# Kernel tuning notes

Measured on AMD Instinct MI355X. Metric: run time of the kernel, lower is better.

Reference implementation:

```python
import jax, jax.numpy as jnp
from jax import lax
import numpy as np

B, Tf, C, D = 4, 128, 8, 64     # batch, frames (num_tokens), animals, input_dim
E, H, L, O = 512, 8, 6, 256     # n_embd, n_head, n_layer, output_dim
T = Tf * C                      # sequence length = 1024
DH = E // H
EPS = 1e-5


def _ln(x, g, b):
    m = jnp.mean(x, -1, keepdims=True)
    v = jnp.mean((x - m) ** 2, -1, keepdims=True)
    return (x - m) * lax.rsqrt(v + EPS) * g + b


def setup_inputs():
    key = jax.random.key(0)
    ks = jax.random.split(key, 16)
    s = 0.02
    n = lambda k, sh: jax.random.normal(k, sh, jnp.float32) * s
    z = lambda sh: jnp.zeros(sh, jnp.float32)
    o = lambda sh: jnp.ones(sh, jnp.float32)
    return {
        'tokens': jax.random.normal(ks[0], (B, Tf, C, D), jnp.float32),
        'pos': (jnp.arange(B * T) % T).reshape(B, T),
        'mask': o((B, T)),
        'bn_g': o((D,)), 'bn_b': z((D,)),
        'We': n(ks[1], (D, E)), 'be': z((E,)),
        'ln1_g': o((L, E)), 'ln1_b': z((L, E)),
        'ln2_g': o((L, E)), 'ln2_b': z((L, E)),
        'Wq': n(ks[2], (L, E, E)), 'bq': z((L, E)),
        'Wk': n(ks[3], (L, E, E)), 'bk': z((L, E)),
        'Wv': n(ks[4], (L, E, E)), 'bv': z((L, E)),
        'Wo': n(ks[5], (L, E, E)), 'bo': z((L, E)),
        'W1': n(ks[6], (L, E, 4 * E)), 'b1': z((L, 4 * E)),
        'W2': n(ks[7], (L, 4 * E, E)), 'b2': z((L, E)),
        'lnf_g': o((E,)), 'lnf_b': z((E,)),
        'Wp': n(ks[8], (E, O)), 'bp': z((O,)),
        'Wd1': n(ks[9], (O, O)), 'bd1': z((O,)),
        'lnd_g': o((O,)), 'lnd_b': z((O,)),
        'Wd2': n(ks[10], (O, D)), 'bd2': z((D,)),
        'Wf1': n(ks[11], (O, O)), 'bf1': z((O,)),
        'lnfr_g': o((O,)), 'lnfr_b': z((O,)),
        'Wf2': n(ks[12], (O, D * C)), 'bf2': z((D * C,)),
    }


def _forward(tokens, mask, bn_g, bn_b, We, be, ln1_g, ln1_b, ln2_g, ln2_b,
             Wq, bq, Wk, bk, Wv, bv, Wo, bo, W1, b1, W2, b2,
             lnf_g, lnf_b, Wp, bp, Wd1, bd1, lnd_g, lnd_b, Wd2, bd2,
             Wf1, bf1, lnfr_g, lnfr_b, Wf2, bf2):
    # BatchNorm2d over feature channel D (training-mode batch stats, biased var)
    mu = jnp.mean(tokens, axis=(0, 1, 2))
    var = jnp.mean((tokens - mu) ** 2, axis=(0, 1, 2))
    tn = (tokens - mu) * lax.rsqrt(var + EPS) * bn_g + bn_b
    x0 = (tn @ We + be).reshape(B, T, E)  # token embeddings, [B,T,E]

    # static block-causal mask: causal over frames, all-to-all within a frame
    static = jnp.kron(jnp.tril(jnp.ones((Tf, Tf), jnp.float32)),
                      jnp.ones((C, C), jnp.float32))  # [T,T]

    def run_blocks(x, dyn):  # dyn: [B,T] key-mask
        allow = (static[None, None] * dyn[:, None, None, :]) > 0  # [B,1,T,T]

        def step(x, p):
            l1g, l1b, wq, bq_, wk, bk_, wv, bv_, wo, bo_, l2g, l2b, w1, b1_, w2, b2_ = p
            h = _ln(x, l1g, l1b)
            q = (h @ wq + bq_).reshape(B, T, H, DH)
            k = (h @ wk + bk_).reshape(B, T, H, DH)
            v = (h @ wv + bv_).reshape(B, T, H, DH)
            att = jnp.einsum('bthd,bshd->bhts', q, k) / jnp.sqrt(jnp.float32(DH))
            att = jnp.where(allow, att, -jnp.inf)
            att = jax.nn.softmax(att, axis=-1)
            y = jnp.einsum('bhts,bshd->bthd', att, v).reshape(B, T, E)
            x = x + y @ wo + bo_
            h2 = _ln(x, l2g, l2b)
            x = x + jax.nn.gelu(h2 @ w1 + b1_, approximate=False) @ w2 + b2_
            return x, None

        x, _ = lax.scan(step, x, (ln1_g, ln1_b, Wq, bq, Wk, bk, Wv, bv, Wo, bo,
                                  ln2_g, ln2_b, W1, b1, W2, b2))
        return x

    x = run_blocks(x0, mask)
    x = _ln(x, lnf_g, lnf_b) @ Wp + bp                 # [B,T,O]
    x2 = run_blocks(x0[:, ::-1], mask[:, ::-1])
    x2 = _ln(x2, lnf_g, lnf_b) @ Wp + bp

    toks = tokens.reshape(B, T, D) * mask[:, :, None]

    def decoder(z):
        h = jnp.tanh(z @ Wd1 + bd1)
        return _ln(h, lnd_g, lnd_b) @ Wd2 + bd2

    def frame_decoder(z):
        h = jnp.tanh(z @ Wf1 + bf1)
        return _ln(h, lnfr_g, lnfr_b) @ Wf2 + bf2

    mse = lambda a, b_: jnp.mean((a - b_) ** 2)
    pred = decoder(x) * mask[:, :, None]
    l_reg = mse(pred[:, :-C], toks[:, C:])
    pred2 = decoder(x2) * mask[:, :, None]
    l_reg_rl = mse(pred2[:, :-C], toks[:, ::-1][:, C:])

    xf = x.reshape(B, Tf, C, O).mean(axis=-2)          # [B,Tf,O]
    l_fr_lr = mse(frame_decoder(xf)[:, :-1], toks.reshape(B, Tf, C * D)[:, 1:])
    xf2 = x2.reshape(B, Tf, C, O).mean(axis=-2)
    l_fr_rl = mse(frame_decoder(xf2)[:, :-1], toks.reshape(B, Tf, C * D)[:, ::-1][:, 1:])

    losses = jnp.stack([l_reg, l_reg_rl, l_fr_lr, l_fr_rl])
    return xf, losses


def reference(tokens, pos, mask, bn_g, bn_b, We, be, ln1_g, ln1_b, ln2_g, ln2_b,
              Wq, bq, Wk, bk, Wv, bv, Wo, bo, W1, b1, W2, b2,
              lnf_g, lnf_b, Wp, bp, Wd1, bd1, lnd_g, lnd_b, Wd2, bd2,
              Wf1, bf1, lnfr_g, lnfr_b, Wf2, bf2):
    # pos is accepted but unused, matching the original forward
    return _forward(tokens, mask, bn_g, bn_b, We, be, ln1_g, ln1_b, ln2_g, ln2_b,
                    Wq, bq, Wk, bk, Wv, bv, Wo, bo, W1, b1, W2, b2,
                    lnf_g, lnf_b, Wp, bp, Wd1, bd1, lnd_g, lnd_b, Wd2, bd2,
                    Wf1, bf1, lnfr_g, lnfr_b, Wf2, bf2)
```

## Files before the change

### kernel.cpp

```cpp
#include <hip/hip_runtime.h>
#include <math.h>

typedef short short8 __attribute__((ext_vector_type(8)));
typedef float f32x4 __attribute__((ext_vector_type(4)));

__device__ __forceinline__ float block_reduce(float v, float* red) {
  int tid = threadIdx.x;
  red[tid] = v; __syncthreads();
  for (int s = 128; s >= 1; s >>= 1) {
    if (tid < s) red[tid] += red[tid + s];
    __syncthreads();
  }
  float r = red[0];
  __syncthreads();
  return r;
}

__device__ __forceinline__ void cvt1(float x, unsigned short& h, unsigned short& l) {
  unsigned u = __float_as_uint(x);
  unsigned hb = (u + 0x8000u) & 0xffff0000u;
  h = (unsigned short)(hb >> 16);
  l = (unsigned short)(__float_as_uint(x - __uint_as_float(hb)) >> 16);
}

__device__ __forceinline__ void cvt2(float a, float b, unsigned& hp, unsigned& lp) {
  unsigned ua = __float_as_uint(a), ub = __float_as_uint(b);
  unsigned ha = (ua + 0x8000u) & 0xffff0000u;
  unsigned hb = (ub + 0x8000u) & 0xffff0000u;
  float la = a - __uint_as_float(ha);
  float lb = b - __uint_as_float(hb);
  hp = (ha >> 16) | hb;
  lp = (__float_as_uint(la) >> 16) | (__float_as_uint(lb) & 0xffff0000u);
}

__device__ __forceinline__ void gl2l(const unsigned short* g, unsigned short* l) {
  __builtin_amdgcn_global_load_lds(
      (const __attribute__((address_space(1))) void*)g,
      (__attribute__((address_space(3))) void*)l, 16, 0, 0);
}

union U8 { unsigned u[4]; short8 s; };

__global__ __launch_bounds__(256) void sentinel_kernel(float* __restrict__ out, int n, float v) {
  int i = blockIdx.x * 256 + threadIdx.x;
  if (i < n) out[i] = v;
}

__global__ __launch_bounds__(256) void bn_stats_kernel(
    const float* __restrict__ tok, const float* __restrict__ g,
    const float* __restrict__ bb, float* __restrict__ ss) {
  __shared__ float red[256];
  const int d = blockIdx.x;
  float sum = 0.f, sumsq = 0.f;
  for (int s = threadIdx.x; s < 4096; s += 256) {
    float v = tok[s * 64 + d];
    sum += v; sumsq += v * v;
  }
  sum = block_reduce(sum, red);
  sumsq = block_reduce(sumsq, red);
  if (threadIdx.x == 0) {
    float mu = sum * (1.f / 4096.f);
    float var = sumsq * (1.f / 4096.f) - mu * mu;
    float sc = g[d] * rsqrtf(fmaxf(var, 0.f) + 1e-5f);
    ss[d] = sc;
    ss[64 + d] = bb[d] - mu * sc;
  }
}

__global__ __launch_bounds__(256) void tn_kernel(
    const float* __restrict__ tok, const float* __restrict__ ss,
    float* __restrict__ tn) {
  int idx = blockIdx.x * 256 + threadIdx.x;
  int d = idx & 63;
  tn[idx] = tok[idx] * ss[d] + ss[64 + d];
}

__global__ __launch_bounds__(256) void reverse_kernel(
    const float* __restrict__ x0, float* __restrict__ x0r) {
  int idx = blockIdx.x * 256 + threadIdx.x;
  int row = idx >> 9, e = idx & 511;
  int b = row >> 10, t = row & 1023;
  x0r[idx] = x0[((size_t)((b << 10) + (1023 - t))) * 512 + e];
}

__global__ __launch_bounds__(256) void ln_kernel(
    const float* __restrict__ x, const float* __restrict__ g,
    const float* __restrict__ b, float* __restrict__ out, int N) {
  __shared__ float red[256];
  const size_t r = blockIdx.x;
  const int tid = threadIdx.x;
  float v0 = x[r * N + tid];
  float v1 = (N > 256) ? x[r * N + 256 + tid] : 0.f;
  float sum = block_reduce(v0 + v1, red);
  float sumsq = block_reduce(v0 * v0 + v1 * v1, red);
  float mean = sum / (float)N;
  float var = sumsq / (float)N - mean * mean;
  float rs = rsqrtf(fmaxf(var, 0.f) + 1e-5f);
  out[r * N + tid] = (v0 - mean) * rs * g[tid] + b[tid];
  if (N > 256)
    out[r * N + 256 + tid] = (v1 - mean) * rs * g[256 + tid] + b[256 + tid];
}

__global__ __launch_bounds__(256) void ln_pl(
    const float* __restrict__ x, const float* __restrict__ g,
    const float* __restrict__ b, unsigned short* __restrict__ oh,
    unsigned short* __restrict__ ol) {
  __shared__ float red[256];
  const size_t r = blockIdx.x;
  const int tid = threadIdx.x;
  float v0 = x[r * 512 + tid];
  float v1 = x[r * 512 + 256 + tid];
  float sum = block_reduce(v0 + v1, red);
  float sumsq = block_reduce(v0 * v0 + v1 * v1, red);
  float mean = sum * (1.f / 512.f);
  float var = sumsq * (1.f / 512.f) - mean * mean;
  float rs = rsqrtf(fmaxf(var, 0.f) + 1e-5f);
  float o0 = (v0 - mean) * rs * g[tid] + b[tid];
  float o1 = (v1 - mean) * rs * g[256 + tid] + b[256 + tid];
  unsigned short h0, l0, h1, l1;
  cvt1(o0, h0, l0); cvt1(o1, h1, l1);
  oh[r * 512 + tid] = h0;       ol[r * 512 + tid] = l0;
  oh[r * 512 + 256 + tid] = h1; ol[r * 512 + 256 + tid] = l1;
}

__global__ __launch_bounds__(256) void convw(
    const float* __restrict__ W, unsigned short* __restrict__ hi,
    unsigned short* __restrict__ lo, int K, int N, long dls) {
  int id = blockIdx.x * 256 + threadIdx.x;
  int total = (K >> 3) * N;
  if (id >= total) return;
  int c = id / N, n = id - c * N;
  const float* Wp = W + (size_t)blockIdx.y * K * N;
  size_t doff = (size_t)blockIdx.y * dls + (size_t)n * K + c * 8;
  unsigned short h8[8], l8[8];
#pragma unroll
  for (int j = 0; j < 8; ++j) {
    float xv = Wp[(size_t)(c * 8 + j) * N + n];
    cvt1(xv, h8[j], l8[j]);
  }
  uint4 hv = make_uint4(h8[0] | ((unsigned)h8[1] << 16), h8[2] | ((unsigned)h8[3] << 16),
                        h8[4] | ((unsigned)h8[5] << 16), h8[6] | ((unsigned)h8[7] << 16));
  uint4 lv = make_uint4(l8[0] | ((unsigned)l8[1] << 16), l8[2] | ((unsigned)l8[3] << 16),
                        l8[4] | ((unsigned)l8[5] << 16), l8[6] | ((unsigned)l8[7] << 16));
  *reinterpret_cast<uint4*>(hi + doff) = hv;
  *reinterpret_cast<uint4*>(lo + doff) = lv;
}

#define BK 16
template <int ACT>
__global__ __launch_bounds__(256) void gemm3(
    const float* __restrict__ A, const float* __restrict__ W,
    const float* __restrict__ bias, const float* resid,
    float* out, int M, int N, int K) {
  __shared__ float As[BK][64 + 4];
  __shared__ float Bs[BK][64 + 4];
  const int tid = threadIdx.x;
  const int tx = tid & 15, ty = tid >> 4;
  const int n0 = blockIdx.x * 64, m0 = blockIdx.y * 64;
  float acc[4][4] = {};
  for (int k0 = 0; k0 < K; k0 += BK) {
    {
      int m = tid >> 2, kq = tid & 3;
      float4 a4 = *reinterpret_cast<const float4*>(A + (size_t)(m0 + m) * K + k0 + kq * 4);
      As[kq * 4 + 0][m] = a4.x; As[kq * 4 + 1][m] = a4.y;
      As[kq * 4 + 2][m] = a4.z; As[kq * 4 + 3][m] = a4.w;
    }
    {
      int kk = tid >> 4, nq = tid & 15;
      float4 b4 = *reinterpret_cast<const float4*>(W + (size_t)(k0 + kk) * N + n0 + nq * 4);
      Bs[kk][nq * 4 + 0] = b4.x; Bs[kk][nq * 4 + 1] = b4.y;
      Bs[kk][nq * 4 + 2] = b4.z; Bs[kk][nq * 4 + 3] = b4.w;
    }
    __syncthreads();
#pragma unroll
    for (int kq = 0; kq < BK; ++kq) {
      float4 av = *reinterpret_cast<const float4*>(&As[kq][ty * 4]);
      float4 bv = *reinterpret_cast<const float4*>(&Bs[kq][tx * 4]);
      acc[0][0] += av.x * bv.x; acc[0][1] += av.x * bv.y; acc[0][2] += av.x * bv.z; acc[0][3] += av.x * bv.w;
      acc[1][0] += av.y * bv.x; acc[1][1] += av.y * bv.y; acc[1][2] += av.y * bv.z; acc[1][3] += av.y * bv.w;
      acc[2][0] += av.z * bv.x; acc[2][1] += av.z * bv.y; acc[2][2] += av.z * bv.z; acc[2][3] += av.z * bv.w;
      acc[3][0] += av.w * bv.x; acc[3][1] += av.w * bv.y; acc[3][2] += av.w * bv.z; acc[3][3] += av.w * bv.w;
    }
    __syncthreads();
  }
#pragma unroll
  for (int i = 0; i < 4; ++i) {
    int m = m0 + ty * 4 + i;
#pragma unroll
    for (int j = 0; j < 4; ++j) {
      int n = n0 + tx * 4 + j;
      float v = acc[i][j] + bias[n];
      if (resid) v += resid[(size_t)m * N + n];
      if (ACT == 1) v = 0.5f * v * (1.f + erff(v * 0.70710678118654752f));
      if (ACT == 2) v = tanhf(v);
      out[(size_t)m * N + n] = v;
    }
  }
}

template <int ACT, int OUTMODE, int ATOMIC, int BIAS3, int QKV>
__global__ __launch_bounds__(256, 2) void gemm_bf(
    const unsigned short* __restrict__ Ahp, const unsigned short* __restrict__ Alp,
    const unsigned short* __restrict__ Bhp, const unsigned short* __restrict__ Blp,
    const float* __restrict__ b0, const float* __restrict__ b1, const float* __restrict__ b2,
    float* __restrict__ Cf, unsigned short* __restrict__ Chp, unsigned short* __restrict__ Clp,
    unsigned short* __restrict__ vth, unsigned short* __restrict__ vtl,
    int M, int N, int K, int KZ) {
  __shared__ __align__(16) unsigned short LDS[2][4][128][32];
  const int tid = threadIdx.x;
  const int lane = tid & 63, wid = tid >> 6;
  const int wr = wid >> 1, wc = wid & 1;
  const int lr = lane & 15, lq = lane >> 4;

  const int gx = gridDim.x;
  int lin = blockIdx.y * gx + blockIdx.x;
  int qch = (gx * gridDim.y) >> 3;
  int swz = (lin & 7) * qch + (lin >> 3);
  const int nb = swz % gx, mb = swz / gx;
  const int n0 = nb * 128, m0 = mb * 128;
  const int kbase = blockIdx.z * KZ, kend = kbase + KZ;

  f32x4 acc[4][4];
#pragma unroll
  for (int i = 0; i < 4; ++i)
#pragma unroll
    for (int j = 0; j < 4; ++j) { acc[i][j][0] = 0.f; acc[i][j][1] = 0.f; acc[i][j][2] = 0.f; acc[i][j][3] = 0.f; }

  const unsigned short* gplane =
      (wid == 0) ? Ahp + (size_t)m0 * K :
      (wid == 1) ? Alp + (size_t)m0 * K :
      (wid == 2) ? Bhp + (size_t)n0 * K : Blp + (size_t)n0 * K;
  const int srow = lane >> 2;
  const int sphys = lane & 3;

  auto stage = [&](int buf, int k0) {
#pragma unroll
    for (int j = 0; j < 8; ++j) {
      int row = j * 16 + srow;
      int logslot = sphys ^ ((row >> 1) & 3);
      gl2l(gplane + (size_t)row * K + k0 + logslot * 8, &LDS[buf][wid][j * 16][0]);
    }
  };

  stage(0, kbase);
  __syncthreads();
  int cur = 0;
  for (int k0 = kbase; k0 < kend; k0 += 32) {
    if (k0 + 32 < kend) stage(cur ^ 1, k0 + 32);
    short8 ah[4], al[4], bh[4], bl[4];
#pragma unroll
    for (int mi = 0; mi < 4; ++mi) {
      int row = wr * 64 + mi * 16 + lr;
      int off = (lq ^ ((row >> 1) & 3)) * 8;
      ah[mi] = *reinterpret_cast<const short8*>(&LDS[cur][0][row][off]);
      al[mi] = *reinterpret_cast<const short8*>(&LDS[cur][1][row][off]);
    }
#pragma unroll
    for (int ni = 0; ni < 4; ++ni) {
      int n = wc * 64 + ni * 16 + lr;
      int off = (lq ^ ((n >> 1) & 3)) * 8;
      bh[ni] = *reinterpret_cast<const short8*>(&LDS[cur][2][n][off]);
      bl[ni] = *reinterpret_cast<const short8*>(&LDS[cur][3][n][off]);
    }
#pragma unroll
    for (int mi = 0; mi < 4; ++mi)
#pragma unroll
      for (int ni = 0; ni < 4; ++ni) {
        acc[mi][ni] = __builtin_amdgcn_mfma_f32_16x16x32_bf16(ah[mi], bh[ni], acc[mi][ni], 0, 0, 0);
        acc[mi][ni] = __builtin_amdgcn_mfma_f32_16x16x32_bf16(ah[mi], bl[ni], acc[mi][ni], 0, 0, 0);
        acc[mi][ni] = __builtin_amdgcn_mfma_f32_16x16x32_bf16(al[mi], bh[ni], acc[mi][ni], 0, 0, 0);
      }
    __syncthreads();
    cur ^= 1;
  }

  if (QKV) {
    const float* bsec = (n0 < 512) ? b0 : (n0 < 1024 ? b1 : b2);
    const int bof = (n0 & 511) - n0;
    if (n0 < 1024) {
      const float scale = (n0 < 512) ? 0.125f : 1.f;
#pragma unroll
      for (int mi = 0; mi < 4; ++mi)
#pragma unroll
        for (int r = 0; r < 4; ++r) {
          int grow = m0 + wr * 64 + mi * 16 + lq * 4 + r;
#pragma unroll
          for (int ni = 0; ni < 4; ++ni) {
            int col = n0 + wc * 64 + ni * 16 + lr;
            float v = (acc[mi][ni][r] + bsec[col + bof]) * scale;
            unsigned short hv, lv;
            cvt1(v, hv, lv);
            Chp[(size_t)grow * N + col] = hv;
            Clp[(size_t)grow * N + col] = lv;
          }
        }
    } else {
#pragma unroll
      for (int mi = 0; mi < 4; ++mi) {
        int t0 = m0 + wr * 64 + mi * 16 + lq * 4;
        int bb = t0 >> 10, tt = t0 & 1023;
#pragma unroll
        for (int ni = 0; ni < 4; ++ni) {
          int col = n0 + wc * 64 + ni * 16 + lr;
          float bias = bsec[col + bof];
          int hh_ = (col - 1024) >> 6, dd = (col - 1024) & 63;
          unsigned short h4[4], l4[4];
#pragma unroll
          for (int r = 0; r < 4; ++r) cvt1(acc[mi][ni][r] + bias, h4[r], l4[r]);
          size_t off = ((size_t)((bb * 8 + hh_) * 64 + dd)) * 1024 + tt;
          *reinterpret_cast<uint2*>(vth + off) = make_uint2(
              h4[0] | ((unsigned)h4[1] << 16), h4[2] | ((unsigned)h4[3] << 16));
          *reinterpret_cast<uint2*>(vtl + off) = make_uint2(
              l4[0] | ((unsigned)l4[1] << 16), l4[2] | ((unsigned)l4[3] << 16));
        }
      }
    }
    return;
  }
  const float* bsec = b0;
  int bof = 0;
  if (BIAS3) { bsec = (n0 < 512) ? b0 : (n0 < 1024 ? b1 : b2); bof = (n0 & 511) - n0; }
#pragma unroll
  for (int mi = 0; mi < 4; ++mi) {
#pragma unroll
    for (int r = 0; r < 4; ++r) {
      int grow = m0 + wr * 64 + mi * 16 + lq * 4 + r;
#pragma unroll
      for (int ni = 0; ni < 4; ++ni) {
        int col = n0 + wc * 64 + ni * 16 + lr;
        float v = acc[mi][ni][r];
        float bias = BIAS3 ? bsec[col + bof] : b0[col];
        if (ATOMIC) {
          if (blockIdx.z == 0) v += bias;
          atomicAdd(&Cf[(size_t)grow * N + col], v);
        } else {
          v += bias;
          if (ACT == 1) v = 0.5f * v * (1.f + erff(v * 0.70710678118654752f));
          if (ACT == 2) v = tanhf(v);
          if (OUTMODE == 0 || OUTMODE == 2) Cf[(size_t)grow * N + col] = v;
          if (OUTMODE >= 1) {
            unsigned short hv, lv;
            cvt1(v, hv, lv);
            Chp[(size_t)grow * N + col] = hv;
            Clp[(size_t)grow * N + col] = lv;
          }
        }
      }
    }
  }
}

__global__ __launch_bounds__(256, 3) void attn_mfma(
    const unsigned short* __restrict__ qkvh, const unsigned short* __restrict__ qkvl,
    const unsigned short* __restrict__ vth, const unsigned short* __restrict__ vtl,
    const float* __restrict__ mask,
    unsigned short* __restrict__ ybh, unsigned short* __restrict__ ybl, int rev) {
  __shared__ __align__(16) unsigned short QK[2][4096];
  __shared__ __align__(16) unsigned short VT[2][4096];
  __shared__ float PU[64 * 68];
  __shared__ float km[64];

  const int tid = threadIdx.x;
  const int lane = tid & 63, w = tid >> 6;
  const int lr = lane & 15, lq = lane >> 4;

  const int id = blockIdx.x;
  const int top = id >> 8;
  const int r5 = id & 255;
  const int qt = top ? (15 - (r5 >> 4)) : (r5 >> 4);
  const int bh_ = (r5 & 15) | (top << 4);
  const int b = bh_ >> 3, h = bh_ & 7;

  {
    const unsigned short* src = (w < 2) ? qkvh : qkvl;
    unsigned short* dst = QK[w >> 1];
    int half = w & 1;
#pragma unroll
    for (int j = 0; j < 4; ++j) {
      int chunk = half * 256 + j * 64 + lane;
      int row = chunk >> 3, p = chunk & 7;
      int slot = p ^ (row & 7);
      gl2l(src + (size_t)(b * 1024 + qt * 64 + row) * 1536 + h * 64 + slot * 8,
           dst + (half * 256 + j * 64) * 8);
    }
  }
  __syncthreads();
  short8 qa_h[2], qa_l[2];
#pragma unroll
  for (int ks = 0; ks < 2; ++ks) {
    int row = w * 16 + lr;
    int phys = (lq + ks * 4) ^ (row & 7);
    qa_h[ks] = *reinterpret_cast<const short8*>(&QK[0][row * 64 + phys * 8]);
    qa_l[ks] = *reinterpret_cast<const short8*>(&QK[1][row * 64 + phys * 8]);
  }
  __syncthreads();

  float m_[4], l_[4] = {0.f, 0.f, 0.f, 0.f};
  f32x4 o_[4];
#pragma unroll
  for (int r = 0; r < 4; ++r) m_[r] = -1e30f;
#pragma unroll
  for (int df = 0; df < 4; ++df) { o_[df][0] = 0.f; o_[df][1] = 0.f; o_[df][2] = 0.f; o_[df][3] = 0.f; }

  for (int kt = 0; kt <= qt; ++kt) {
    if (w < 2) {
      const unsigned short* src = (w == 0) ? qkvh : qkvl;
      unsigned short* dst = QK[w];
#pragma unroll
      for (int j = 0; j < 8; ++j) {
        int chunk = j * 64 + lane;
        int row = chunk >> 3, p = chunk & 7;
        int slot = p ^ (row & 7);
        gl2l(src + (size_t)(b * 1024 + kt * 64 + row) * 1536 + 512 + h * 64 + slot * 8,
             dst + j * 512);
      }
    } else {
      const unsigned short* src = (w == 2) ? vth : vtl;
      unsigned short* dst = VT[w - 2];
#pragma unroll
      for (int j = 0; j < 8; ++j) {
        int chunk = j * 64 + lane;
        int row = chunk >> 3, p = chunk & 7;
        int slot = p ^ (row & 7);
        gl2l(src + (size_t)((b * 8 + h) * 64 + row) * 1024 + kt * 64 + slot * 8,
             dst + j * 512);
      }
    }
    if (tid < 64) {
      int s = kt * 64 + tid;
      km[tid] = mask[b * 1024 + (rev ? (1023 - s) : s)];
    }
    __syncthreads();

    f32x4 sacc[4];
#pragma unroll
    for (int kf = 0; kf < 4; ++kf) { sacc[kf][0] = 0.f; sacc[kf][1] = 0.f; sacc[kf][2] = 0.f; sacc[kf][3] = 0.f; }
#pragma unroll
    for (int ks = 0; ks < 2; ++ks) {
#pragma unroll
      for (int kf = 0; kf < 4; ++kf) {
        int col = kf * 16 + lr;
        int phys = (lq + ks * 4) ^ (lr & 7);
        short8 kbh = *reinterpret_cast<const short8*>(&QK[0][col * 64 + phys * 8]);
        short8 kbl = *reinterpret_cast<const short8*>(&QK[1][col * 64 + phys * 8]);
        sacc[kf] = __builtin_amdgcn_mfma_f32_16x16x32_bf16(qa_h[ks], kbh, sacc[kf], 0, 0, 0);
        sacc[kf] = __builtin_amdgcn_mfma_f32_16x16x32_bf16(qa_h[ks], kbl, sacc[kf], 0, 0, 0);
        sacc[kf] = __builtin_amdgcn_mfma_f32_16x16x32_bf16(qa_l[ks], kbh, sacc[kf], 0, 0, 0);
      }
    }

    const bool diag = (kt == qt);
    float kmv[4];
#pragma unroll
    for (int kf = 0; kf < 4; ++kf) kmv[kf] = km[kf * 16 + lr];
#pragma unroll
    for (int r = 0; r < 4; ++r) {
      int fi = (w * 16 + lq * 4 + r) >> 3;
      float mt = -1e30f;
#pragma unroll
      for (int kf = 0; kf < 4; ++kf) {
        int key = kf * 16 + lr;
        bool ok = (kmv[kf] > 0.f) && (!diag || ((key >> 3) <= fi));
        float x = ok ? sacc[kf][r] : -1e30f;
        sacc[kf][r] = x;
        mt = fmaxf(mt, x);
      }
      mt = fmaxf(mt, __shfl_xor(mt, 1, 16));
      mt = fmaxf(mt, __shfl_xor(mt, 2, 16));
      mt = fmaxf(mt, __shfl_xor(mt, 4, 16));
      mt = fmaxf(mt, __shfl_xor(mt, 8, 16));
      float mn = fmaxf(m_[r], mt);
      float al = __expf(m_[r] - mn);
      m_[r] = mn;
      float rs = 0.f;
#pragma unroll
      for (int kf = 0; kf < 4; ++kf) {
        float sv = sacc[kf][r];
        float p = (sv > -1e29f) ? __expf(sv - mn) : 0.f;
        sacc[kf][r] = p;
        rs += p;
      }
      rs += __shfl_xor(rs, 1, 16);
      rs += __shfl_xor(rs, 2, 16);
      rs += __shfl_xor(rs, 4, 16);
      rs += __shfl_xor(rs, 8, 16);
      l_[r] = l_[r] * al + rs;
#pragma unroll
      for (int df = 0; df < 4; ++df) o_[df][r] *= al;
    }
#pragma unroll
    for (int kf = 0; kf < 4; ++kf)
#pragma unroll
      for (int r = 0; r < 4; ++r)
        PU[(w * 16 + lq * 4 + r) * 68 + kf * 16 + lr] = sacc[kf][r];
    __syncthreads();

#pragma unroll
    for (int ks = 0; ks < 2; ++ks) {
      const float* pp = &PU[(w * 16 + lr) * 68 + ks * 32 + lq * 8];
      float4 p0 = *reinterpret_cast<const float4*>(pp);
      float4 p1 = *reinterpret_cast<const float4*>(pp + 4);
      U8 th, tl;
      cvt2(p0.x, p0.y, th.u[0], tl.u[0]);
      cvt2(p0.z, p0.w, th.u[1], tl.u[1]);
      cvt2(p1.x, p1.y, th.u[2], tl.u[2]);
      cvt2(p1.z, p1.w, th.u[3], tl.u[3]);
      short8 pa_h = th.s, pa_l = tl.s;
#pragma unroll
      for (int df = 0; df < 4; ++df) {
        int col = df * 16 + lr;
        int phys = (lq + ks * 4) ^ (lr & 7);
        short8 vbh = *reinterpret_cast<const short8*>(&VT[0][col * 64 + phys * 8]);
        short8 vbl = *reinterpret_cast<const short8*>(&VT[1][col * 64 + phys * 8]);
        o_[df] = __builtin_amdgcn_mfma_f32_16x16x32_bf16(pa_h, vbh, o_[df], 0, 0, 0);
        o_[df] = __builtin_amdgcn_mfma_f32_16x16x32_bf16(pa_h, vbl, o_[df], 0, 0, 0);
        o_[df] = __builtin_amdgcn_mfma_f32_16x16x32_bf16(pa_l, vbh, o_[df], 0, 0, 0);
      }
    }
    __syncthreads();
  }

#pragma unroll
  for (int r = 0; r < 4; ++r) {
    float inv = 1.f / fmaxf(l_[r], 1e-30f);
    int qrow = qt * 64 + w * 16 + lq * 4 + r;
#pragma unroll
    for (int df = 0; df < 4; ++df) {
      float val = o_[df][r] * inv;
      unsigned short hv, lv;
      cvt1(val, hv, lv);
      size_t idx = (size_t)(b * 1024 + qrow) * 512 + h * 64 + df * 16 + lr;
      ybh[idx] = hv; ybl[idx] = lv;
    }
  }
}

__global__ __launch_bounds__(256) void frame_mean_kernel(
    const float* __restrict__ xo, float* __restrict__ xf,
    float* __restrict__ outf) {
  int row = blockIdx.x;
  int o = threadIdx.x;
  float s = 0.f;
#pragma unroll
  for (int c = 0; c < 8; ++c) s += xo[((size_t)row * 8 + c) * 256 + o];
  s *= 0.125f;
  xf[row * 256 + o] = s;
  if (outf) outf[row * 256 + o] = s;
}

__global__ __launch_bounds__(256) void loss_reg_kernel(
    const float* __restrict__ pd, const float* __restrict__ tok,
    const float* __restrict__ mask, float* __restrict__ acc, int rev) {
  __shared__ float red[256];
  float local = 0.f;
  for (int idx = blockIdx.x * 256 + threadIdx.x; idx < 260096; idx += gridDim.x * 256) {
    int b = idx / 65024, r2 = idx % 65024;
    int t = r2 >> 6, d = r2 & 63;
    float pred = pd[((size_t)((b << 10) + t)) * 64 + d] * mask[(b << 10) + t];
    int tt = rev ? (1015 - t) : (t + 8);
    float tgt = tok[((size_t)((b << 10) + tt)) * 64 + d] * mask[(b << 10) + tt];
    float df = pred - tgt;
    local += df * df;
  }
  float s = block_reduce(local, red);
  if (threadIdx.x == 0) atomicAdd(acc, s);
}

__global__ __launch_bounds__(256) void loss_fr_kernel(
    const float* __restrict__ pf, const float* __restrict__ tok,
    const float* __restrict__ mask, float* __restrict__ acc, int rev) {
  __shared__ float red[256];
  float local = 0.f;
  for (int idx = blockIdx.x * 256 + threadIdx.x; idx < 260096; idx += gridDim.x * 256) {
    int b = idx / 65024, r2 = idx % 65024;
    int i = r2 >> 9, u = r2 & 511;
    float pred = pf[((size_t)(b * 128 + i)) * 512 + u];
    int c = u >> 6;
    int t = rev ? ((126 - i) * 8 + c) : ((i + 1) * 8 + c);
    float tgt = tok[((size_t)((b << 10) + t)) * 64 + (u & 63)] * mask[(b << 10) + t];
    float df = pred - tgt;
    local += df * df;
  }
  float s = block_reduce(local, red);
  if (threadIdx.x == 0) atomicAdd(acc, s);
}

__global__ void finalize_kernel(const float* __restrict__ acc, float* __restrict__ out) {
  int i = threadIdx.x;
  if (i < 4) out[131072 + i] = acc[i] * (1.0f / 260096.0f);
}

extern "C" void kernel_launch(void* const* d_in, const int* in_sizes, int n_in,
                              void* d_out, int out_size, void* d_ws, size_t ws_size,
                              hipStream_t stream) {
  float* ws = (float*)d_ws;
  const size_t OFF_SS   = 0;
  const size_t OFF_LACC = 128;
  const size_t OFF_TN   = 256;
  const size_t OFF_X0   = 262400;
  const size_t OFF_X0R  = 2359552;
  const size_t OFF_X    = 4456704;
  const size_t OFF_HPL  = 6553856;
  const size_t OFF_QKV  = 8651008;
  const size_t OFF_YB   = 14942464;
  const size_t OFF_XO   = 17039616;
  const size_t OFF_XOPL = 18088192;
  const size_t OFF_HD   = 19136768;
  const size_t OFF_HD2  = 20185344;
  const size_t OFF_PD   = 21233920;
  const size_t OFF_XF   = 21496064;
  const size_t OFF_HF   = 21627136;
  const size_t OFF_HF2  = 21758208;
  const size_t OFF_PF   = 21889280;
  const size_t OFF_VT   = 22151424;
  const size_t OFF_WB   = 24248576;
  const size_t TOTAL_MIN = OFF_WB + 1048576;
  const size_t TOTAL_BIG = OFF_WB + 19070976;

  float* ss   = ws + OFF_SS;
  float* lacc = ws + OFF_LACC;
  float* tn   = ws + OFF_TN;
  float* x0   = ws + OFF_X0;
  float* x0r  = ws + OFF_X0R;
  float* x    = ws + OFF_X;
  unsigned short* hh = (unsigned short*)(ws + OFF_HPL);
  unsigned short* hl = hh + 2097152;
  unsigned short* qkvh = (unsigned short*)(ws + OFF_QKV);
  unsigned short* qkvl = qkvh + 6291456;
  unsigned short* uh = (unsigned short*)(ws + OFF_QKV);
  unsigned short* ul = uh + 8388608;
  unsigned short* ybh = (unsigned short*)(ws + OFF_YB);
  unsigned short* ybl = ybh + 2097152;
  float* xo   = ws + OFF_XO;
  unsigned short* xoh = (unsigned short*)(ws + OFF_XOPL);
  unsigned short* xol = xoh + 1048576;
  float* hd   = ws + OFF_HD;
  float* hd2  = ws + OFF_HD2;
  float* pd   = ws + OFF_PD;
  float* xf   = ws + OFF_XF;
  float* hf   = ws + OFF_HF;
  float* hf2  = ws + OFF_HF2;
  float* pf   = ws + OFF_PF;
  unsigned short* vth = (unsigned short*)(ws + OFF_VT);
  unsigned short* vtl = vth + 2097152;
  unsigned short* wb16 = (unsigned short*)(ws + OFF_WB);
  float* out_f = (float*)d_out;

  static const int EXPECTED[39] = {
      262144, 4096, 4096, 64, 64, 32768, 512, 3072, 3072, 3072, 3072,
      1572864, 3072, 1572864, 3072, 1572864, 3072, 1572864, 3072,
      6291456, 12288, 6291456, 3072, 512, 512, 131072, 256, 65536, 256,
      256, 256, 16384, 64, 65536, 256, 256, 256, 131072, 512};
  bool manifest_ok = (n_in == 39) && (ws_size >= TOTAL_MIN * sizeof(float));
  if (manifest_ok)
    for (int i = 0; i < 39; ++i)
      if (in_sizes[i] != EXPECTED[i]) { manifest_ok = false; break; }
  if (!manifest_ok) {
    hipLaunchKernelGGL(sentinel_kernel, dim3((out_size + 255) / 256), dim3(256), 0, stream,
                       out_f, out_size, 2000.0f);
    return;
  }
  const bool bigws = ws_size >= TOTAL_BIG * sizeof(float);

  const float* tok    = (const float*)d_in[0];
  const float* mask   = (const float*)d_in[2];
  const float* bn_g   = (const float*)d_in[3];
  const float* bn_b   = (const float*)d_in[4];
  const float* We     = (const float*)d_in[5];
  const float* be     = (const float*)d_in[6];
  const float* ln1_g  = (const float*)d_in[7];
  const float* ln1_b  = (const float*)d_in[8];
  const float* ln2_g  = (const float*)d_in[9];
  const float* ln2_b  = (const float*)d_in[10];
  const float* Wq     = (const float*)d_in[11];
  const float* bq     = (const float*)d_in[12];
  const float* Wk     = (const float*)d_in[13];
  const float* bk     = (const float*)d_in[14];
  const float* Wv     = (const float*)d_in[15];
  const float* bv     = (const float*)d_in[16];
  const float* Wo     = (const float*)d_in[17];
  const float* bo     = (const float*)d_in[18];
  const float* W1     = (const float*)d_in[19];
  const float* b1     = (const float*)d_in[20];
  const float* W2     = (const float*)d_in[21];
  const float* b2     = (const float*)d_in[22];
  const float* lnf_g  = (const float*)d_in[23];
  const float* lnf_b  = (const float*)d_in[24];
  const float* Wp     = (const float*)d_in[25];
  const float* bp     = (const float*)d_in[26];
  const float* Wd1    = (const float*)d_in[27];
  const float* bd1    = (const float*)d_in[28];
  const float* lnd_g  = (const float*)d_in[29];
  const float* lnd_b  = (const float*)d_in[30];
  const float* Wd2    = (const float*)d_in[31];
  const float* bd2    = (const float*)d_in[32];
  const float* Wf1    = (const float*)d_in[33];
  const float* bf1    = (const float*)d_in[34];
  const float* lnfr_g = (const float*)d_in[35];
  const float* lnfr_b = (const float*)d_in[36];
  const float* Wf2    = (const float*)d_in[37];
  const float* bf2    = (const float*)d_in[38];

  unsigned short* wqkv_h = wb16;
  unsigned short* wqkv_l = wb16 + 4718592;
  unsigned short* wo_h   = wb16 + 9437184;
  unsigned short* wo_l   = wb16 + 11010048;
  unsigned short* w1_h   = wb16 + 12582912;
  unsigned short* w1_l   = wb16 + 18874368;
  unsigned short* w2_h   = wb16 + 25165824;
  unsigned short* w2_l   = wb16 + 31457280;
  unsigned short* wp_h   = wb16 + 37748736;
  unsigned short* wp_l   = wb16 + 37879808;
  unsigned short* wd1_h  = wb16 + 38010880;
  unsigned short* wd1_l  = wb16 + 38076416;
  unsigned short* scr    = wb16;

  auto G = [&](int act, const float* A, const float* W, const float* bias,
               const float* resid, float* out, int M, int N, int K) {
    dim3 g(N / 64, M / 64), b(256);
    if (act == 0) hipLaunchKernelGGL((gemm3<0>), g, b, 0, stream, A, W, bias, resid, out, M, N, K);
    else if (act == 1) hipLaunchKernelGGL((gemm3<1>), g, b, 0, stream, A, W, bias, resid, out, M, N, K);
    else hipLaunchKernelGGL((gemm3<2>), g, b, 0, stream, A, W, bias, resid, out, M, N, K);
  };
  auto CONV = [&](const float* W, unsigned short* hi, unsigned short* lo,
                  int K, int N, int layers, long dls) {
    int blocks = ((K >> 3) * N + 255) / 256;
    hipLaunchKernelGGL(convw, dim3(blocks, layers), dim3(256), 0, stream, W, hi, lo, K, N, dls);
  };

  hipMemsetAsync(lacc, 0, 4 * sizeof(float), stream);
  if (bigws) {
    CONV(Wq, wqkv_h,          wqkv_l,          512, 512, 6, 786432);
    CONV(Wk, wqkv_h + 262144, wqkv_l + 262144, 512, 512, 6, 786432);
    CONV(Wv, wqkv_h + 524288, wqkv_l + 524288, 512, 512, 6, 786432);
    CONV(Wo, wo_h, wo_l, 512, 512, 6, 262144);
    CONV(W1, w1_h, w1_l, 512, 2048, 6, 1048576);
    CONV(W2, w2_h, w2_l, 2048, 512, 6, 1048576);
    CONV(Wp, wp_h, wp_l, 512, 256, 1, 0);
    CONV(Wd1, wd1_h, wd1_l, 256, 256, 1, 0);
  }
  hipLaunchKernelGGL(bn_stats_kernel, dim3(64), dim3(256), 0, stream, tok, bn_g, bn_b, ss);
  hipLaunchKernelGGL(tn_kernel, dim3(1024), dim3(256), 0, stream, tok, ss, tn);
  G(0, tn, We, be, nullptr, x0, 4096, 512, 64);
  hipLaunchKernelGGL(reverse_kernel, dim3(8192), dim3(256), 0, stream, x0, x0r);

  for (int dir = 0; dir < 2; ++dir) {
    const float* xin = dir ? x0r : x0;
    for (int l = 0; l < 6; ++l) {
      const float* xl = (l == 0) ? xin : x;
      hipLaunchKernelGGL(ln_pl, dim3(4096), dim3(256), 0, stream,
                         xl, ln1_g + l * 512, ln1_b + l * 512, hh, hl);
      const unsigned short *pqh, *pql;
      if (bigws) { pqh = wqkv_h + (size_t)l * 786432; pql = wqkv_l + (size_t)l * 786432; }
      else {
        CONV(Wq + (size_t)l * 262144, scr,          scr + 786432,          512, 512, 1, 0);
        CONV(Wk + (size_t)l * 262144, scr + 262144, scr + 786432 + 262144, 512, 512, 1, 0);
        CONV(Wv + (size_t)l * 262144, scr + 524288, scr + 786432 + 524288, 512, 512, 1, 0);
        pqh = scr; pql = scr + 786432;
      }
      hipLaunchKernelGGL((gemm_bf<0, 1, 0, 1, 1>), dim3(12, 32, 1), dim3(256), 0, stream,
                         hh, hl, pqh, pql, bq + l * 512, bk + l * 512, bv + l * 512,
                         nullptr, qkvh, qkvl, vth, vtl, 4096, 1536, 512, 512);
      if (l == 0)
        hipMemcpyAsync(x, xin, 2097152 * sizeof(float), hipMemcpyDeviceToDevice, stream);
      hipLaunchKernelGGL(attn_mfma, dim3(512), dim3(256), 0, stream,
                         qkvh, qkvl, vth, vtl, mask, ybh, ybl, dir);
      const unsigned short *poh, *pol;
      if (bigws) { poh = wo_h + (size_t)l * 262144; pol = wo_l + (size_t)l * 262144; }
      else {
        CONV(Wo + (size_t)l * 262144, scr, scr + 262144, 512, 512, 1, 0);
        poh = scr; pol = scr + 262144;
      }
      hipLaunchKernelGGL((gemm_bf<0, 0, 1, 0, 0>), dim3(4, 32, 2), dim3(256), 0, stream,
                         ybh, ybl, poh, pol, bo + l * 512, nullptr, nullptr,
                         x, nullptr, nullptr, nullptr, nullptr, 4096, 512, 512, 256);
      hipLaunchKernelGGL(ln_pl, dim3(4096), dim3(256), 0, stream,
                         x, ln2_g + l * 512, ln2_b + l * 512, hh, hl);
      const unsigned short *p1h, *p1l;
      if (bigws) { p1h = w1_h + (size_t)l * 1048576; p1l = w1_l + (size_t)l * 1048576; }
      else {
        CONV(W1 + (size_t)l * 1048576, scr, scr + 1048576, 512, 2048, 1, 0);
        p1h = scr; p1l = scr + 1048576;
      }
      hipLaunchKernelGGL((gemm_bf<1, 1, 0, 0, 0>), dim3(16, 32, 1), dim3(256), 0, stream,
                         hh, hl, p1h, p1l, b1 + l * 2048, nullptr, nullptr,
                         nullptr, uh, ul, nullptr, nullptr, 4096, 2048, 512, 512);
      const unsigned short *p2h, *p2l;
      if (bigws) { p2h = w2_h + (size_t)l * 1048576; p2l = w2_l + (size_t)l * 1048576; }
      else {
        CONV(W2 + (size_t)l * 1048576, scr, scr + 1048576, 2048, 512, 1, 0);
        p2h = scr; p2l = scr + 1048576;
      }
      hipLaunchKernelGGL((gemm_bf<0, 0, 1, 0, 0>), dim3(4, 32, 2), dim3(256), 0, stream,
                         uh, ul, p2h, p2l, b2 + l * 512, nullptr, nullptr,
                         x, nullptr, nullptr, nullptr, nullptr, 4096, 512, 2048, 1024);
    }
    hipLaunchKernelGGL(ln_pl, dim3(4096), dim3(256), 0, stream, x, lnf_g, lnf_b, hh, hl);
    const unsigned short *pph, *ppl, *pdh, *pdl;
    if (bigws) { pph = wp_h; ppl = wp_l; }
    else { CONV(Wp, scr, scr + 131072, 512, 256, 1, 0); pph = scr; ppl = scr + 131072; }
    hipLaunchKernelGGL((gemm_bf<0, 2, 0, 0, 0>), dim3(2, 32, 1), dim3(256), 0, stream,
                       hh, hl, pph, ppl, bp, nullptr, nullptr,
                       xo, xoh, xol, nullptr, nullptr, 4096, 256, 512, 512);
    if (bigws) { pdh = wd1_h; pdl = wd1_l; }
    else { CONV(Wd1, scr, scr + 65536, 256, 256, 1, 0); pdh = scr; pdl = scr + 65536; }
    hipLaunchKernelGGL((gemm_bf<2, 0, 0, 0, 0>), dim3(2, 32, 1), dim3(256), 0, stream,
                       xoh, xol, pdh, pdl, bd1, nullptr, nullptr,
                       hd, nullptr, nullptr, nullptr, nullptr, 4096, 256, 256, 256);
    hipLaunchKernelGGL(ln_kernel, dim3(4096), dim3(256), 0, stream, hd, lnd_g, lnd_b, hd2, 256);
    G(0, hd2, Wd2, bd2, nullptr, pd, 4096, 64, 256);
    hipLaunchKernelGGL(loss_reg_kernel, dim3(256), dim3(256), 0, stream,
                       pd, tok, mask, lacc + (dir ? 1 : 0), dir);
    hipLaunchKernelGGL(frame_mean_kernel, dim3(512), dim3(256), 0, stream,
                       xo, xf, dir == 0 ? out_f : (float*)nullptr);
    G(2, xf, Wf1, bf1, nullptr, hf, 512, 256, 256);
    hipLaunchKernelGGL(ln_kernel, dim3(512), dim3(256), 0, stream, hf, lnfr_g, lnfr_b, hf2, 256);
    G(0, hf2, Wf2, bf2, nullptr, pf, 512, 512, 256);
    hipLaunchKernelGGL(loss_fr_kernel, dim3(256), dim3(256), 0, stream,
                       pf, tok, mask, lacc + (dir ? 3 : 2), dir);
  }
  hipLaunchKernelGGL(finalize_kernel, dim3(1), dim3(64), 0, stream, lacc, out_f);
}
```

Before: 2.733 ms.

## Double-buffer K tiles in attention and make LayerNorm warp-per-row

The attention kernel now keeps two K buffers in LDS and prefetches the next K tile while the current one is processed. The V tile load is issued at the start of each iteration. Mask values are read straight from global memory, which removes the shared km array and one barrier per iteration, and the Q staging area now reuses the PU scratch space. The extra LDS lowers the launch-bounds occupancy hint from 3 blocks to 2. Separately, the pre-GEMM LayerNorm now uses one wavefront per row with float4 loads, shuffle reductions and packed 128-bit stores instead of a shared-memory block reduction, so it launches 8× fewer blocks.

After: 2.566 ms. 6.1% less time.

```diff
diff --git a/kernel.cpp b/kernel.cpp
--- a/kernel.cpp
+++ b/kernel.cpp
@@ -105,22 +105,45 @@
     const float* __restrict__ x, const float* __restrict__ g,
     const float* __restrict__ b, unsigned short* __restrict__ oh,
     unsigned short* __restrict__ ol) {
-  __shared__ float red[256];
-  const size_t r = blockIdx.x;
-  const int tid = threadIdx.x;
-  float v0 = x[r * 512 + tid];
-  float v1 = x[r * 512 + 256 + tid];
-  float sum = block_reduce(v0 + v1, red);
-  float sumsq = block_reduce(v0 * v0 + v1 * v1, red);
-  float mean = sum * (1.f / 512.f);
-  float var = sumsq * (1.f / 512.f) - mean * mean;
-  float rs = rsqrtf(fmaxf(var, 0.f) + 1e-5f);
-  float o0 = (v0 - mean) * rs * g[tid] + b[tid];
-  float o1 = (v1 - mean) * rs * g[256 + tid] + b[256 + tid];
-  unsigned short h0, l0, h1, l1;
-  cvt1(o0, h0, l0); cvt1(o1, h1, l1);
-  oh[r * 512 + tid] = h0;       ol[r * 512 + tid] = l0;
-  oh[r * 512 + 256 + tid] = h1; ol[r * 512 + 256 + tid] = l1;
+  const int w = threadIdx.x >> 6, lane = threadIdx.x & 63;
+  const int c0 = lane * 8;
+  float4 g0 = *reinterpret_cast<const float4*>(g + c0);
+  float4 g1 = *reinterpret_cast<const float4*>(g + c0 + 4);
+  float4 b0 = *reinterpret_cast<const float4*>(b + c0);
+  float4 b1 = *reinterpret_cast<const float4*>(b + c0 + 4);
+  const float gv[8] = {g0.x, g0.y, g0.z, g0.w, g1.x, g1.y, g1.z, g1.w};
+  const float bv[8] = {b0.x, b0.y, b0.z, b0.w, b1.x, b1.y, b1.z, b1.w};
+#pragma unroll
+  for (int rr = 0; rr < 2; ++rr) {
+    size_t r = (size_t)blockIdx.x * 8 + w * 2 + rr;
+    const float* xp = x + r * 512 + c0;
+    float4 a0 = *reinterpret_cast<const float4*>(xp);
+    float4 a1 = *reinterpret_cast<const float4*>(xp + 4);
+    const float av[8] = {a0.x, a0.y, a0.z, a0.w, a1.x, a1.y, a1.z, a1.w};
+    float s = 0.f, q = 0.f;
+#pragma unroll
+    for (int j = 0; j < 8; ++j) { s += av[j]; q += av[j] * av[j]; }
+#pragma unroll
+    for (int off = 32; off >= 1; off >>= 1) {
+      s += __shfl_xor(s, off);
+      q += __shfl_xor(q, off);
+    }
+    float mean = s * (1.f / 512.f);
+    float var = q * (1.f / 512.f) - mean * mean;
+    float rs = rsqrtf(fmaxf(var, 0.f) + 1e-5f);
+    unsigned short hv[8], lv[8];
+#pragma unroll
+    for (int j = 0; j < 8; ++j) {
+      float o = (av[j] - mean) * rs * gv[j] + bv[j];
+      cvt1(o, hv[j], lv[j]);
+    }
+    uint4 hq = make_uint4(hv[0] | ((unsigned)hv[1] << 16), hv[2] | ((unsigned)hv[3] << 16),
+                          hv[4] | ((unsigned)hv[5] << 16), hv[6] | ((unsigned)hv[7] << 16));
+    uint4 lq = make_uint4(lv[0] | ((unsigned)lv[1] << 16), lv[2] | ((unsigned)lv[3] << 16),
+                          lv[4] | ((unsigned)lv[5] << 16), lv[6] | ((unsigned)lv[7] << 16));
+    *reinterpret_cast<uint4*>(oh + r * 512 + c0) = hq;
+    *reinterpret_cast<uint4*>(ol + r * 512 + c0) = lq;
+  }
 }
 
 __global__ __launch_bounds__(256) void convw(
@@ -350,15 +373,14 @@
   }
 }
 
-__global__ __launch_bounds__(256, 3) void attn_mfma(
+__global__ __launch_bounds__(256, 2) void attn_mfma(
     const unsigned short* __restrict__ qkvh, const unsigned short* __restrict__ qkvl,
     const unsigned short* __restrict__ vth, const unsigned short* __restrict__ vtl,
     const float* __restrict__ mask,
     unsigned short* __restrict__ ybh, unsigned short* __restrict__ ybl, int rev) {
-  __shared__ __align__(16) unsigned short QK[2][4096];
-  __shared__ __align__(16) unsigned short VT[2][4096];
-  __shared__ float PU[64 * 68];
-  __shared__ float km[64];
+  __shared__ __align__(16) unsigned short KB[2][2][4096];
+  __shared__ __align__(16) unsigned short VB[2][4096];
+  __shared__ __align__(16) float PU[64 * 68];
 
   const int tid = threadIdx.x;
   const int lane = tid & 63, w = tid >> 6;
@@ -371,9 +393,34 @@
   const int bh_ = (r5 & 15) | (top << 4);
   const int b = bh_ >> 3, h = bh_ & 7;
 
+  const int srow = lane >> 3, sp = lane & 7;
+  auto stageK = [&](int buf, int kt2) {
+    const unsigned short* src = (w == 0) ? qkvh : qkvl;
+    unsigned short* dst = &KB[buf][w][0];
+#pragma unroll
+    for (int j = 0; j < 8; ++j) {
+      int row = j * 8 + srow;
+      int slot = sp ^ (row & 7);
+      gl2l(src + (size_t)(b * 1024 + kt2 * 64 + row) * 1536 + 512 + h * 64 + slot * 8,
+           dst + j * 512);
+    }
+  };
+  auto stageV = [&](int kt2) {
+    const unsigned short* src = (w == 2) ? vth : vtl;
+    unsigned short* dst = &VB[w - 2][0];
+#pragma unroll
+    for (int j = 0; j < 8; ++j) {
+      int row = j * 8 + srow;
+      int slot = sp ^ (row & 7);
+      gl2l(src + (size_t)((b * 8 + h) * 64 + row) * 1024 + kt2 * 64 + slot * 8,
+           dst + j * 512);
+    }
+  };
+
+  unsigned short* QS = reinterpret_cast<unsigned short*>(PU);
   {
     const unsigned short* src = (w < 2) ? qkvh : qkvl;
-    unsigned short* dst = QK[w >> 1];
+    unsigned short* dst = QS + (w >> 1) * 4096;
     int half = w & 1;
 #pragma unroll
     for (int j = 0; j < 4; ++j) {
@@ -384,14 +431,15 @@
            dst + (half * 256 + j * 64) * 8);
     }
   }
+  if (w < 2) stageK(0, 0);
   __syncthreads();
   short8 qa_h[2], qa_l[2];
 #pragma unroll
   for (int ks = 0; ks < 2; ++ks) {
     int row = w * 16 + lr;
     int phys = (lq + ks * 4) ^ (row & 7);
-    qa_h[ks] = *reinterpret_cast<const short8*>(&QK[0][row * 64 + phys * 8]);
-    qa_l[ks] = *reinterpret_cast<const short8*>(&QK[1][row * 64 + phys * 8]);
+    qa_h[ks] = *reinterpret_cast<const short8*>(&QS[row * 64 + phys * 8]);
+    qa_l[ks] = *reinterpret_cast<const short8*>(&QS[4096 + row * 64 + phys * 8]);
   }
   __syncthreads();
 
@@ -402,35 +450,16 @@
 #pragma unroll
   for (int df = 0; df < 4; ++df) { o_[df][0] = 0.f; o_[df][1] = 0.f; o_[df][2] = 0.f; o_[df][3] = 0.f; }
 
+  int cur = 0;
   for (int kt = 0; kt <= qt; ++kt) {
-    if (w < 2) {
-      const unsigned short* src = (w == 0) ? qkvh : qkvl;
-      unsigned short* dst = QK[w];
-#pragma unroll
-      for (int j = 0; j < 8; ++j) {
-        int chunk = j * 64 + lane;
-        int row = chunk >> 3, p = chunk & 7;
-        int slot = p ^ (row & 7);
-        gl2l(src + (size_t)(b * 1024 + kt * 64 + row) * 1536 + 512 + h * 64 + slot * 8,
-             dst + j * 512);
-      }
-    } else {
-      const unsigned short* src = (w == 2) ? vth : vtl;
-      unsigned short* dst = VT[w - 2];
-#pragma unroll
-      for (int j = 0; j < 8; ++j) {
-        int chunk = j * 64 + lane;
-        int row = chunk >> 3, p = chunk & 7;
-        int slot = p ^ (row & 7);
-        gl2l(src + (size_t)((b * 8 + h) * 64 + row) * 1024 + kt * 64 + slot * 8,
-             dst + j * 512);
-      }
-    }
-    if (tid < 64) {
-      int s = kt * 64 + tid;
-      km[tid] = mask[b * 1024 + (rev ? (1023 - s) : s)];
-    }
-    __syncthreads();
+    if (w < 2) { if (kt < qt) stageK(cur ^ 1, kt + 1); }
+    else stageV(kt);
+    float kmv[4];
+#pragma unroll
+    for (int kf = 0; kf < 4; ++kf) {
+      int s = kt * 64 + kf * 16 + lr;
+      kmv[kf] = mask[b * 1024 + (rev ? (1023 - s) : s)];
+    }
 
     f32x4 sacc[4];
 #pragma unroll
@@ -441,8 +470,8 @@
       for (int kf = 0; kf < 4; ++kf) {
         int col = kf * 16 + lr;
         int phys = (lq + ks * 4) ^ (lr & 7);
-        short8 kbh = *reinterpret_cast<const short8*>(&QK[0][col * 64 + phys * 8]);
-        short8 kbl = *reinterpret_cast<const short8*>(&QK[1][col * 64 + phys * 8]);
+        short8 kbh = *reinterpret_cast<const short8*>(&KB[cur][0][col * 64 + phys * 8]);
+        short8 kbl = *reinterpret_cast<const short8*>(&KB[cur][1][col * 64 + phys * 8]);
         sacc[kf] = __builtin_amdgcn_mfma_f32_16x16x32_bf16(qa_h[ks], kbh, sacc[kf], 0, 0, 0);
         sacc[kf] = __builtin_amdgcn_mfma_f32_16x16x32_bf16(qa_h[ks], kbl, sacc[kf], 0, 0, 0);
         sacc[kf] = __builtin_amdgcn_mfma_f32_16x16x32_bf16(qa_l[ks], kbh, sacc[kf], 0, 0, 0);
@@ -450,9 +479,6 @@
     }
 
     const bool diag = (kt == qt);
-    float kmv[4];
-#pragma unroll
-    for (int kf = 0; kf < 4; ++kf) kmv[kf] = km[kf * 16 + lr];
 #pragma unroll
     for (int r = 0; r < 4; ++r) {
       int fi = (w * 16 + lq * 4 + r) >> 3;
@@ -510,14 +536,15 @@
       for (int df = 0; df < 4; ++df) {
         int col = df * 16 + lr;
         int phys = (lq + ks * 4) ^ (lr & 7);
-        short8 vbh = *reinterpret_cast<const short8*>(&VT[0][col * 64 + phys * 8]);
-        short8 vbl = *reinterpret_cast<const short8*>(&VT[1][col * 64 + phys * 8]);
+        short8 vbh = *reinterpret_cast<const short8*>(&VB[0][col * 64 + phys * 8]);
+        short8 vbl = *reinterpret_cast<const short8*>(&VB[1][col * 64 + phys * 8]);
         o_[df] = __builtin_amdgcn_mfma_f32_16x16x32_bf16(pa_h, vbh, o_[df], 0, 0, 0);
         o_[df] = __builtin_amdgcn_mfma_f32_16x16x32_bf16(pa_h, vbl, o_[df], 0, 0, 0);
         o_[df] = __builtin_amdgcn_mfma_f32_16x16x32_bf16(pa_l, vbh, o_[df], 0, 0, 0);
       }
     }
     __syncthreads();
+    cur ^= 1;
   }
 
 #pragma unroll
@@ -748,7 +775,7 @@
     const float* xin = dir ? x0r : x0;
     for (int l = 0; l < 6; ++l) {
       const float* xl = (l == 0) ? xin : x;
-      hipLaunchKernelGGL(ln_pl, dim3(4096), dim3(256), 0, stream,
+      hipLaunchKernelGGL(ln_pl, dim3(512), dim3(256), 0, stream,
                          xl, ln1_g + l * 512, ln1_b + l * 512, hh, hl);
       const unsigned short *pqh, *pql;
       if (bigws) { pqh = wqkv_h + (size_t)l * 786432; pql = wqkv_l + (size_t)l * 786432; }
@@ -774,7 +801,7 @@
       hipLaunchKernelGGL((gemm_bf<0, 0, 1, 0, 0>), dim3(4, 32, 2), dim3(256), 0, stream,
                          ybh, ybl, poh, pol, bo + l * 512, nullptr, nullptr,
                          x, nullptr, nullptr, nullptr, nullptr, 4096, 512, 512, 256);
-      hipLaunchKernelGGL(ln_pl, dim3(4096), dim3(256), 0, stream,
+      hipLaunchKernelGGL(ln_pl, dim3(512), dim3(256), 0, stream,
                          x, ln2_g + l * 512, ln2_b + l * 512, hh, hl);
       const unsigned short *p1h, *p1l;
       if (bigws) { p1h = w1_h + (size_t)l * 1048576; p1l = w1_l + (size_t)l * 1048576; }
@@ -795,7 +822,7 @@
                          uh, ul, p2h, p2l, b2 + l * 512, nullptr, nullptr,
                          x, nullptr, nullptr, nullptr, nullptr, 4096, 512, 2048, 1024);
     }
-    hipLaunchKernelGGL(ln_pl, dim3(4096), dim3(256), 0, stream, x, lnf_g, lnf_b, hh, hl);
+    hipLaunchKernelGGL(ln_pl, dim3(512), dim3(256), 0, stream, x, lnf_g, lnf_b, hh, hl);
     const unsigned short *pph, *ppl, *pdh, *pdl;
     if (bigws) { pph = wp_h; ppl = wp_l; }
     else { CONV(Wp, scr, scr + 131072, 512, 256, 1, 0); pph = scr; ppl = scr + 131072; }
```
